# Performance work log

Measured on AMD Instinct MI355X. Metric: run time of the kernel, lower is better.

Reference implementation:

```python
import jax, jax.numpy as jnp
import numpy as np

PI = float(np.pi)


def _apply_acts(a, x):
    """Vectorized per-node activation dispatch.
    a: [n] int activation ids (applyAct lookup table), x: [B, n].
    Matches torch applyAct: ids 2..11 select a function, anything else is identity.
    """
    A = a[None, :]  # broadcast over batch
    v = x  # actId 1 / default: identity
    v = jnp.where(A == 2, (x > 0.0).astype(x.dtype), v)           # unsigned step
    v = jnp.where(A == 3, jnp.sin(PI * x), v)                      # sin
    v = jnp.where(A == 4, jnp.exp(-0.5 * x * x), v)                # gaussian
    v = jnp.where(A == 5, jnp.tanh(x), v)                          # tanh
    v = jnp.where(A == 6, 0.5 * (jnp.tanh(0.5 * x) + 1.0), v)      # sigmoid
    v = jnp.where(A == 7, -x, v)                                   # inverse
    v = jnp.where(A == 8, jnp.abs(x), v)                           # abs
    v = jnp.where(A == 9, jnp.maximum(0.0, x), v)                  # relu
    v = jnp.where(A == 10, jnp.cos(PI * x), v)                     # cos
    v = jnp.where(A == 11, x * x, v)                               # squared
    return v


def setup_inputs() -> dict:
    key = jax.random.key(0)
    ks = jax.random.split(key, 10)
    B, nIn, H1, H2, nOut = 65536, 256, 256, 256, 128
    SPARSITY = 0.5  # fraction of zeroed connections, like a WANN sparse topology

    def sparse_w(kw, km, shape):
        w = jax.random.normal(kw, shape, jnp.float32)
        keep = jax.random.uniform(km, shape) > SPARSITY
        return w * keep.astype(jnp.float32)

    x = jax.random.normal(ks[0], (B, nIn), jnp.float32)
    W0 = sparse_w(ks[1], ks[2], (nIn + 1, H1))  # layer0 (bias+inputs) -> layer1
    W1 = sparse_w(ks[3], ks[4], (H1, H2))       # layer1 -> layer2
    W2 = sparse_w(ks[5], ks[6], (H2, nOut))     # layer2 -> output layer
    a1 = jax.random.randint(ks[7], (H1,), 0, 12).astype(jnp.int32)
    a2 = jax.random.randint(ks[8], (H2,), 0, 12).astype(jnp.int32)
    a3 = jax.random.randint(ks[9], (nOut,), 0, 12).astype(jnp.int32)
    return {"x": x, "W0": W0, "W1": W1, "W2": W2, "a1": a1, "a2": a2, "a3": a3}


def reference(x, W0, W1, W2, a1, a2, a3):
    B = x.shape[0]
    # layer 0 activations: bias node (=1) followed by the inputs
    h = jnp.concatenate([jnp.ones((B, 1), x.dtype), x], axis=1)  # [B, nIn+1]
    # each SparseLinear is (weight * mask) matmul; mask = weight != 0
    h = _apply_acts(a1, h @ (W0 * (W0 != 0)))  # [B, H1]
    h = _apply_acts(a2, h @ (W1 * (W1 != 0)))  # [B, H2]
    h = _apply_acts(a3, h @ (W2 * (W2 != 0)))  # [B, nOut]
    return h  # all_activations[:, -nOutput:] == final layer
```

## Files before the change

kernel.cpp:

```cpp
#include <hip/hip_runtime.h>
#include <hip/hip_bf16.h>
#include <math.h>

typedef __attribute__((ext_vector_type(8)))  short short8;
typedef __attribute__((ext_vector_type(16))) float f32x16;

constexpr int TB = 32;
constexpr int PLANE = 16384;

__device__ __forceinline__ float vexp2f(float x) {
    float r; asm("v_exp_f32 %0, %1" : "=v"(r) : "v"(x)); return r;
}

__device__ __forceinline__ unsigned int bf16_rne_bits(float x) {
    unsigned int u = __float_as_uint(x);
    return (u + 0x7fffu + ((u >> 16) & 1u)) & 0xffff0000u;
}
__device__ __forceinline__ void split3(float x, unsigned short& h, unsigned short& m, unsigned short& l) {
    const unsigned int hb = bf16_rne_bits(x);
    const float r1 = x - __uint_as_float(hb);
    const unsigned int mb = bf16_rne_bits(r1);
    const float r2 = r1 - __uint_as_float(mb);
    h = (unsigned short)(hb >> 16);
    m = (unsigned short)(mb >> 16);
    l = (unsigned short)(__float_as_uint(r2) >> 16);
}

__device__ __forceinline__ float apply_act(int a, float x) {
    const float x2 = x * x;
    const float roff = (a == 10) ? 0.25f : 0.0f;
    const float r  = __builtin_amdgcn_fractf(fmaf(0.5f, x, roff));
    const float sn = __builtin_amdgcn_sinf(r);
    const float eop = (a == 4) ? x2 : x;
    const float ecf = (a == 4) ? -0.72134752044448169f
                               : ((a == 5) ? 2.8853900817779268f : -1.4426950408889634f);
    const float e  = vexp2f(eop * ecf);
    const float d  = __builtin_amdgcn_rcpf(1.0f + e);
    float ev = d;
    ev = (a == 4) ? e : ev;
    ev = (a == 5) ? fmaf(-2.0f, d, 1.0f) : ev;
    float v = x;
    v = (a == 2)  ? (x > 0.0f ? 1.0f : 0.0f) : v;
    v = (a == 3 || a == 10) ? sn : v;
    v = (a >= 4 && a <= 6)  ? ev : v;
    v = (a == 7)  ? -x : v;
    v = (a == 8)  ? fabsf(x) : v;
    v = (a == 9)  ? fmaxf(0.0f, x) : v;
    v = (a == 11) ? x2 : v;
    return v;
}

__global__ void pack_w(const float* __restrict__ W0, const float* __restrict__ W1,
                       const float* __restrict__ W2, unsigned short* __restrict__ ws) {
    const int g = blockIdx.x;
    const int lane = threadIdx.x;
    const int hi = lane >> 5, ln31 = lane & 31;
    const float* W; int t, c, ldw, rowoff;
    if (g < 128)      { W = W0; t = g >> 3;        c = g & 7;        ldw = 256; rowoff = 1; }
    else if (g < 256) { W = W1; t = (g-128) >> 3;  c = (g-128) & 7;  ldw = 256; rowoff = 0; }
    else              { W = W2; t = (g-256) >> 2;  c = (g-256) & 3;  ldw = 128; rowoff = 0; }
    const int col = c * 32 + ln31;
    unsigned short hb[8], mb[8], lb[8];
    #pragma unroll
    for (int i = 0; i < 8; ++i) {
        const int k = t * 16 + hi * 8 + i;
        split3(W[(size_t)(rowoff + k) * ldw + col], hb[i], mb[i], lb[i]);
    }
    size_t base = ((size_t)(g * 3 + 0) * 64 + lane) * 8;
    #pragma unroll
    for (int i = 0; i < 8; ++i) ws[base + i] = hb[i];
    base += 64 * 8;
    #pragma unroll
    for (int i = 0; i < 8; ++i) ws[base + i] = mb[i];
    base += 64 * 8;
    #pragma unroll
    for (int i = 0; i < 8; ++i) ws[base + i] = lb[i];
}

template<int NC_TOT>
__device__ __forceinline__ void gemm_layer(const short8* __restrict__ wsL, const char* smem,
                                           f32x16& acc, int ctile, int lane) {
    const int hi = lane >> 5, ln31 = lane & 31;
    const int abase = ln31 * 512;
    const int swzm = (ln31 & 7) << 4;
    const short8* bp = wsL + (size_t)ctile * 192 + lane;
    #pragma unroll 2
    for (int t = 0; t < 16; ++t) {
        const int koff = abase + ((t * 32 + hi * 16) ^ swzm);
        short8 ah = *(const short8*)(smem + 0 * PLANE + koff);
        short8 am = *(const short8*)(smem + 1 * PLANE + koff);
        short8 al = *(const short8*)(smem + 2 * PLANE + koff);
        short8 bh = bp[0];
        short8 bm = bp[64];
        short8 bl = bp[128];
        bp += NC_TOT * 192;
        acc = __builtin_amdgcn_mfma_f32_32x32x16_bf16(ah, bh, acc, 0, 0, 0);
        acc = __builtin_amdgcn_mfma_f32_32x32x16_bf16(ah, bm, acc, 0, 0, 0);
        acc = __builtin_amdgcn_mfma_f32_32x32x16_bf16(am, bh, acc, 0, 0, 0);
        acc = __builtin_amdgcn_mfma_f32_32x32x16_bf16(ah, bl, acc, 0, 0, 0);
        acc = __builtin_amdgcn_mfma_f32_32x32x16_bf16(am, bm, acc, 0, 0, 0);
        acc = __builtin_amdgcn_mfma_f32_32x32x16_bf16(al, bh, acc, 0, 0, 0);
    }
}

__device__ __forceinline__ void act_store_lds(const f32x16& acc, const int* __restrict__ act,
                                              char* smem, int ctile, int lane) {
    const int hi = lane >> 5, ln31 = lane & 31;
    const int col = ctile * 32 + ln31;
    const int aid = act[col];
    const int kbyte = 2 * col;
    __syncthreads();
    #pragma unroll
    for (int rr = 0; rr < 16; ++rr) {
        const float v = apply_act(aid, acc[rr]);
        const int row = (rr & 3) + 8 * (rr >> 2) + 4 * hi;
        const int addr = row * 512 + (kbyte ^ ((row & 7) << 4));
        unsigned short h, m, l;
        split3(v, h, m, l);
        *(unsigned short*)(smem + 0 * PLANE + addr) = h;
        *(unsigned short*)(smem + 1 * PLANE + addr) = m;
        *(unsigned short*)(smem + 2 * PLANE + addr) = l;
    }
    __syncthreads();
}

__global__ __launch_bounds__(512, 6)
void wann_mfma(const float* __restrict__ x,
               const float* __restrict__ W0,
               const unsigned short* __restrict__ ws,
               const int* __restrict__ a1, const int* __restrict__ a2,
               const int* __restrict__ a3,
               float* __restrict__ out) {
    extern __shared__ char smem[];
    const int tid = threadIdx.x;
    const int lane = tid & 63;
    const int wid = tid >> 6;
    const int ln31 = lane & 31;
    const int hi = lane >> 5;
    const int row0 = blockIdx.x * TB;

    {
        const float4* xv = (const float4*)(x + (size_t)row0 * 256);
        #pragma unroll
        for (int p = 0; p < 4; ++p) {
            const int f = p * 512 + tid;
            const int r = f >> 6;
            const int swz = (r & 7) << 4;
            const int kb0 = (f & 63) * 8;
            const float4 v = xv[f];
            const float vv[4] = {v.x, v.y, v.z, v.w};
            #pragma unroll
            for (int e = 0; e < 4; ++e) {
                unsigned short h, m, l;
                split3(vv[e], h, m, l);
                const int addr = r * 512 + ((kb0 + 2 * e) ^ swz);
                *(unsigned short*)(smem + 0 * PLANE + addr) = h;
                *(unsigned short*)(smem + 1 * PLANE + addr) = m;
                *(unsigned short*)(smem + 2 * PLANE + addr) = l;
            }
        }
    }
    __syncthreads();

    const short8* wsv  = (const short8*)ws;
    const short8* wsL0 = wsv;
    const short8* wsL1 = wsv + (size_t)128 * 3 * 64;
    const short8* wsL2 = wsv + (size_t)256 * 3 * 64;

    f32x16 acc;

    {
        const float b = W0[wid * 32 + ln31];
        #pragma unroll
        for (int rr = 0; rr < 16; ++rr) acc[rr] = b;
        gemm_layer<8>(wsL0, smem, acc, wid, lane);
        act_store_lds(acc, a1, smem, wid, lane);
    }

    {
        #pragma unroll
        for (int rr = 0; rr < 16; ++rr) acc[rr] = 0.0f;
        gemm_layer<8>(wsL1, smem, acc, wid, lane);
        act_store_lds(acc, a2, smem, wid, lane);
    }

    if (wid < 4) {
        #pragma unroll
        for (int rr = 0; rr < 16; ++rr) acc[rr] = 0.0f;
        gemm_layer<4>(wsL2, smem, acc, wid, lane);
        const int col = wid * 32 + ln31;
        const int aid = a3[col];
        #pragma unroll
        for (int rr = 0; rr < 16; ++rr) {
            const float v = apply_act(aid, acc[rr]);
            const int orow = (rr & 3) + 8 * (rr >> 2) + 4 * hi;
            out[(size_t)(row0 + orow) * 128 + col] = v;
        }
    }
}

extern "C" void kernel_launch(void* const* d_in, const int* in_sizes, int n_in,
                              void* d_out, int out_size, void* d_ws, size_t ws_size,
                              hipStream_t stream) {
    const float* x  = (const float*)d_in[0];
    const float* W0 = (const float*)d_in[1];
    const float* W1 = (const float*)d_in[2];
    const float* W2 = (const float*)d_in[3];
    const int*   a1 = (const int*)d_in[4];
    const int*   a2 = (const int*)d_in[5];
    const int*   a3 = (const int*)d_in[6];
    float* out = (float*)d_out;

    unsigned short* ws = (unsigned short*)d_ws;

    hipFuncSetAttribute(reinterpret_cast<const void*>(wann_mfma),
                        hipFuncAttributeMaxDynamicSharedMemorySize, 3 * PLANE);

    hipLaunchKernelGGL(pack_w, dim3(320), dim3(64), 0, stream, W0, W1, W2, ws);

    const int B = in_sizes[0] / 256;
    hipLaunchKernelGGL(wann_mfma, dim3(B / TB), dim3(512), 3 * PLANE, stream,
                       x, W0, ws, a1, a2, a3, out);
}
```

Baseline: 227.3 us.

## Prefetch B fragments, use packed bf16 conversion, and widen LDS stores

Weight fragments are now loaded one k-step ahead in the GEMM loop, the loop is fully unrolled, and the MFMA block runs at raised wave priority. The software bf16 split is replaced with the hardware v_cvt_pk_bf16_f32 packed conversion, processing two values at a time, and the input staging writes 64-bit LDS stores instead of 16-bit ones. Activations are computed before the barrier rather than interleaved with the stores. The pack_w kernel is also launched with 4 waves per block. The aim is to hide global-load latency and cut ALU and LDS instruction counts, at the cost of higher register pressure, which could lower occupancy under the 6-wave launch bound. The low residual is now rounded to bf16 instead of truncated, which changes numerics slightly.

```diff
diff --git a/kernel.cpp b/kernel.cpp
--- a/kernel.cpp
+++ b/kernel.cpp
@@ -10,6 +10,24 @@
 
 __device__ __forceinline__ float vexp2f(float x) {
     float r; asm("v_exp_f32 %0, %1" : "=v"(r) : "v"(x)); return r;
+}
+
+__device__ __forceinline__ unsigned int cvtpk_bf16(float a, float b) {
+    unsigned int r;
+    asm("v_cvt_pk_bf16_f32 %0, %1, %2" : "=v"(r) : "v"(a), "v"(b));
+    return r;
+}
+
+__device__ __forceinline__ void split3_pair(float v0, float v1,
+                                            unsigned int& hp, unsigned int& mp, unsigned int& lp) {
+    hp = cvtpk_bf16(v0, v1);
+    const float h0 = __uint_as_float(hp << 16);
+    const float h1 = __uint_as_float(hp & 0xffff0000u);
+    const float r0 = v0 - h0, r1 = v1 - h1;
+    mp = cvtpk_bf16(r0, r1);
+    const float m0 = __uint_as_float(mp << 16);
+    const float m1 = __uint_as_float(mp & 0xffff0000u);
+    lp = cvtpk_bf16(r0 - m0, r1 - m1);
 }
 
 __device__ __forceinline__ unsigned int bf16_rne_bits(float x) {
@@ -52,8 +70,8 @@
 
 __global__ void pack_w(const float* __restrict__ W0, const float* __restrict__ W1,
                        const float* __restrict__ W2, unsigned short* __restrict__ ws) {
-    const int g = blockIdx.x;
-    const int lane = threadIdx.x;
+    const int g = blockIdx.x * 4 + (threadIdx.x >> 6);
+    const int lane = threadIdx.x & 63;
     const int hi = lane >> 5, ln31 = lane & 31;
     const float* W; int t, c, ldw, rowoff;
     if (g < 128)      { W = W0; t = g >> 3;        c = g & 7;        ldw = 256; rowoff = 1; }
@@ -84,22 +102,30 @@
     const int abase = ln31 * 512;
     const int swzm = (ln31 & 7) << 4;
     const short8* bp = wsL + (size_t)ctile * 192 + lane;
-    #pragma unroll 2
+    short8 bh = bp[0];
+    short8 bm = bp[64];
+    short8 bl = bp[128];
+    #pragma unroll
     for (int t = 0; t < 16; ++t) {
         const int koff = abase + ((t * 32 + hi * 16) ^ swzm);
         short8 ah = *(const short8*)(smem + 0 * PLANE + koff);
         short8 am = *(const short8*)(smem + 1 * PLANE + koff);
         short8 al = *(const short8*)(smem + 2 * PLANE + koff);
-        short8 bh = bp[0];
-        short8 bm = bp[64];
-        short8 bl = bp[128];
-        bp += NC_TOT * 192;
+        short8 nbh, nbm, nbl;
+        if (t < 15) {
+            const short8* bn = bp + NC_TOT * 192;
+            nbh = bn[0]; nbm = bn[64]; nbl = bn[128];
+            bp = bn;
+        }
+        __builtin_amdgcn_s_setprio(1);
         acc = __builtin_amdgcn_mfma_f32_32x32x16_bf16(ah, bh, acc, 0, 0, 0);
         acc = __builtin_amdgcn_mfma_f32_32x32x16_bf16(ah, bm, acc, 0, 0, 0);
         acc = __builtin_amdgcn_mfma_f32_32x32x16_bf16(am, bh, acc, 0, 0, 0);
         acc = __builtin_amdgcn_mfma_f32_32x32x16_bf16(ah, bl, acc, 0, 0, 0);
         acc = __builtin_amdgcn_mfma_f32_32x32x16_bf16(am, bm, acc, 0, 0, 0);
         acc = __builtin_amdgcn_mfma_f32_32x32x16_bf16(al, bh, acc, 0, 0, 0);
+        __builtin_amdgcn_s_setprio(0);
+        if (t < 15) { bh = nbh; bm = nbm; bl = nbl; }
     }
 }
 
@@ -109,17 +135,24 @@
     const int col = ctile * 32 + ln31;
     const int aid = act[col];
     const int kbyte = 2 * col;
+    float v[16];
+    #pragma unroll
+    for (int rr = 0; rr < 16; ++rr) v[rr] = apply_act(aid, acc[rr]);
     __syncthreads();
     #pragma unroll
-    for (int rr = 0; rr < 16; ++rr) {
-        const float v = apply_act(aid, acc[rr]);
-        const int row = (rr & 3) + 8 * (rr >> 2) + 4 * hi;
-        const int addr = row * 512 + (kbyte ^ ((row & 7) << 4));
-        unsigned short h, m, l;
-        split3(v, h, m, l);
-        *(unsigned short*)(smem + 0 * PLANE + addr) = h;
-        *(unsigned short*)(smem + 1 * PLANE + addr) = m;
-        *(unsigned short*)(smem + 2 * PLANE + addr) = l;
+    for (int p = 0; p < 8; ++p) {
+        const int rr0 = 2 * p;
+        unsigned int hp, mp, lp;
+        split3_pair(v[rr0], v[rr0 + 1], hp, mp, lp);
+        const int row0 = (rr0 & 3) + 8 * (rr0 >> 2) + 4 * hi;
+        const int a0 = row0 * 512 + (kbyte ^ ((row0 & 7) << 4));
+        const int a1 = (row0 + 1) * 512 + (kbyte ^ (((row0 + 1) & 7) << 4));
+        *(unsigned short*)(smem + 0 * PLANE + a0) = (unsigned short)hp;
+        *(unsigned short*)(smem + 0 * PLANE + a1) = (unsigned short)(hp >> 16);
+        *(unsigned short*)(smem + 1 * PLANE + a0) = (unsigned short)mp;
+        *(unsigned short*)(smem + 1 * PLANE + a1) = (unsigned short)(mp >> 16);
+        *(unsigned short*)(smem + 2 * PLANE + a0) = (unsigned short)lp;
+        *(unsigned short*)(smem + 2 * PLANE + a1) = (unsigned short)(lp >> 16);
     }
     __syncthreads();
 }
@@ -148,16 +181,16 @@
             const int swz = (r & 7) << 4;
             const int kb0 = (f & 63) * 8;
             const float4 v = xv[f];
-            const float vv[4] = {v.x, v.y, v.z, v.w};
-            #pragma unroll
-            for (int e = 0; e < 4; ++e) {
-                unsigned short h, m, l;
-                split3(vv[e], h, m, l);
-                const int addr = r * 512 + ((kb0 + 2 * e) ^ swz);
-                *(unsigned short*)(smem + 0 * PLANE + addr) = h;
-                *(unsigned short*)(smem + 1 * PLANE + addr) = m;
-                *(unsigned short*)(smem + 2 * PLANE + addr) = l;
-            }
+            unsigned int h01, m01, l01, h23, m23, l23;
+            split3_pair(v.x, v.y, h01, m01, l01);
+            split3_pair(v.z, v.w, h23, m23, l23);
+            const int a0 = r * 512 + (kb0 ^ swz);
+            *(unsigned long long*)(smem + 0 * PLANE + a0) =
+                (unsigned long long)h01 | ((unsigned long long)h23 << 32);
+            *(unsigned long long*)(smem + 1 * PLANE + a0) =
+                (unsigned long long)m01 | ((unsigned long long)m23 << 32);
+            *(unsigned long long*)(smem + 2 * PLANE + a0) =
+                (unsigned long long)l01 | ((unsigned long long)l23 << 32);
         }
     }
     __syncthreads();
@@ -216,7 +249,7 @@
     hipFuncSetAttribute(reinterpret_cast<const void*>(wann_mfma),
                         hipFuncAttributeMaxDynamicSharedMemorySize, 3 * PLANE);
 
-    hipLaunchKernelGGL(pack_w, dim3(320), dim3(64), 0, stream, W0, W1, W2, ws);
+    hipLaunchKernelGGL(pack_w, dim3(80), dim3(256), 0, stream, W0, W1, W2, ws);
 
     const int B = in_sizes[0] / 256;
     hipLaunchKernelGGL(wann_mfma, dim3(B / TB), dim3(512), 3 * PLANE, stream,
```

Measured after the change: 239.2 us. 5.2% more time.
